# Kernel tuning notes

Measured on AMD Instinct MI355X. Metric: run time of the kernel, lower is better.

Reference implementation:

```python
import jax, jax.numpy as jnp
import numpy as np


def binarize(t):
    # sign binarizer to exactly +/-1 (sign(0) -> +1), matching is_binary_tensor check
    return jnp.where(t >= 0, 1.0, -1.0).astype(t.dtype)


def setup_inputs() -> dict:
    key = jax.random.key(0)
    kx, kw, kb = jax.random.split(key, 3)
    x = jax.random.normal(kx, (32, 256, 56, 56), dtype=jnp.float32)
    weight = jax.random.normal(kw, (256, 256, 3, 3), dtype=jnp.float32)
    bias = jax.random.normal(kb, (256,), dtype=jnp.float32)
    return {"x": x, "weight": weight, "bias": bias}


def reference(x, weight, bias):
    bx = binarize(x)            # [B, Cin, H, W] in {-1, +1}
    bw = binarize(weight)       # [Cout, Cin, kh, kw] in {-1, +1}
    # F.conv2d(stride=1, padding=1, dilation=1, groups=1)
    out = jax.lax.conv_general_dilated(
        bx, bw,
        window_strides=(1, 1),
        padding=((1, 1), (1, 1)),
        dimension_numbers=("NCHW", "OIHW", "NCHW"),
    )
    return out + bias[None, :, None, None]
```

## Files before the change

kernel.cpp:

```cpp
#include <hip/hip_runtime.h>
#include <cstdint>

constexpr int B = 32, C = 256, H = 56, W = 56;
constexpr int HW = H * W;
constexpr int WORDS = C / 32;
constexpr int TAPS = 9;
constexpr int WPC = TAPS * WORDS;
constexpr int PH = H + 2, PW = W + 2, PHW = PH * PW;

__global__ __launch_bounds__(256) void pack_x_kernel(const float* __restrict__ x,
                                                     uint32_t* __restrict__ px) {
    int idx = blockIdx.x * 256 + threadIdx.x;
    int pp = idx % PHW;
    int r = idx / PHW;
    int wd = r % WORDS;
    int b = r / WORDS;
    int ph = pp / PW, pwp = pp - ph * PW;
    uint32_t bits = 0;
    if (ph >= 1 && ph <= H && pwp >= 1 && pwp <= W) {
        const float* xp = x + ((size_t)b * C + wd * 32) * HW + (size_t)(ph - 1) * W + (pwp - 1);
        #pragma unroll
        for (int i = 0; i < 32; ++i)
            bits |= (xp[(size_t)i * HW] < 0.0f ? (1u << i) : 0u);
    }
    px[((size_t)(b * PH + ph) * PW + pwp) * WORDS + wd] = bits;
}

__global__ __launch_bounds__(256) void pack_w_kernel(const float* __restrict__ wt,
                                                     const float* __restrict__ bias,
                                                     uint32_t* __restrict__ pw,
                                                     float* __restrict__ basep) {
    int idx = blockIdx.x * 256 + threadIdx.x;
    if (idx < C) basep[idx] = 2304.0f + bias[idx];
    if (idx >= C * WPC) return;
    int co = idx / WPC;
    int r = idx - co * WPC;
    int tap = r / WORDS;
    int wd = r - tap * WORDS;
    const float* wp = wt + ((size_t)co * C + wd * 32) * TAPS + tap;
    uint32_t bits = 0;
    #pragma unroll
    for (int i = 0; i < 32; ++i)
        bits |= (wp[(size_t)i * TAPS] < 0.0f ? (1u << i) : 0u);
    pw[(size_t)co * WPC + (size_t)tap * WORDS + wd] = bits;
}

__global__ __launch_bounds__(256) void bconv_kernel(const uint32_t* __restrict__ px,
                                                    const uint32_t* __restrict__ pw,
                                                    const float* __restrict__ basep,
                                                    float* __restrict__ out) {
    const int lane = threadIdx.x & 63;
    const int wid = __builtin_amdgcn_readfirstlane(threadIdx.x >> 6);
    const int hw = blockIdx.x * 64 + lane;
    const int b = blockIdx.y;
    const int h = hw / W;
    const int w = hw - h * W;

    uint32_t pxr[TAPS][WORDS];
    #pragma unroll
    for (int dh = -1; dh <= 1; ++dh) {
        #pragma unroll
        for (int dw = -1; dw <= 1; ++dw) {
            const int t = (dh + 1) * 3 + (dw + 1);
            const uint4* p = reinterpret_cast<const uint4*>(
                px + ((size_t)(b * PH + (h + 1 + dh)) * PW + (w + 1 + dw)) * WORDS);
            uint4 a = p[0], q = p[1];
            pxr[t][0] = a.x; pxr[t][1] = a.y; pxr[t][2] = a.z; pxr[t][3] = a.w;
            pxr[t][4] = q.x; pxr[t][5] = q.y; pxr[t][6] = q.z; pxr[t][7] = q.w;
        }
    }

    const int cobase = wid * 64;
    const uint32_t* wbase = pw + (size_t)cobase * WPC;
    const float* bbase = basep + cobase;
    float* op = out + ((size_t)b * C + cobase) * HW + hw;

    #pragma unroll 1
    for (int j = 0; j < 64; ++j) {
        const uint32_t* wr = wbase + (size_t)j * WPC;
        uint32_t acc[4] = {0u, 0u, 0u, 0u};
        #pragma unroll
        for (int t = 0; t < TAPS; ++t) {
            #pragma unroll
            for (int k = 0; k < WORDS; ++k)
                acc[(t * WORDS + k) & 3] += __popc(pxr[t][k] ^ wr[t * WORDS + k]);
        }
        uint32_t total = (acc[0] + acc[1]) + (acc[2] + acc[3]);
        float res = fmaf(-2.0f, (float)(int)total, bbase[j]);
        op[(size_t)j * HW] = res;
    }
}

__global__ __launch_bounds__(256) void border_kernel(const uint32_t* __restrict__ px,
                                                     const uint32_t* __restrict__ pw,
                                                     const float* __restrict__ bias,
                                                     float* __restrict__ out) {
    int idx = blockIdx.x * 256 + threadIdx.x;
    int e = idx % 220;
    int r = idx / 220;
    int co = r & 255;
    int b = r >> 8;
    int h, w;
    if (e < 56)       { h = 0;            w = e; }
    else if (e < 112) { h = 55;           w = e - 56; }
    else if (e < 166) { h = 1 + (e - 112); w = 0; }
    else              { h = 1 + (e - 166); w = 55; }

    const uint32_t* wr = pw + (size_t)co * WPC;
    uint32_t total = 0;
    int nvalid = 0;
    #pragma unroll
    for (int dh = -1; dh <= 1; ++dh) {
        #pragma unroll
        for (int dw = -1; dw <= 1; ++dw) {
            const int t = (dh + 1) * 3 + (dw + 1);
            const int hh = h + dh, ww = w + dw;
            const bool v = (hh >= 0) & (hh < H) & (ww >= 0) & (ww < W);
            const uint32_t* p = px + ((size_t)(b * PH + (hh + 1)) * PW + (ww + 1)) * WORDS;
            uint32_t pt = 0;
            #pragma unroll
            for (int k = 0; k < WORDS; ++k)
                pt += __popc(p[k] ^ wr[t * WORDS + k]);
            total += v ? pt : 0u;
            nvalid += v ? 1 : 0;
        }
    }
    float res = (float)(256 * nvalid) - 2.0f * (float)(int)total + bias[co];
    out[((size_t)b * C + co) * HW + (size_t)h * W + w] = res;
}

extern "C" void kernel_launch(void* const* d_in, const int* in_sizes, int n_in,
                              void* d_out, int out_size, void* d_ws, size_t ws_size,
                              hipStream_t stream) {
    const float* x = (const float*)d_in[0];
    const float* wt = (const float*)d_in[1];
    const float* bias = (const float*)d_in[2];
    float* out = (float*)d_out;

    uint32_t* px = (uint32_t*)d_ws;
    uint32_t* pw = px + (size_t)B * PHW * WORDS;
    float* basep = (float*)(pw + (size_t)C * WPC);

    pack_x_kernel<<<(B * WORDS * PHW) / 256, 256, 0, stream>>>(x, px);
    pack_w_kernel<<<(C * WPC + 255) / 256, 256, 0, stream>>>(wt, bias, pw, basep);

    dim3 grid(HW / 64, B);
    bconv_kernel<<<grid, 256, 0, stream>>>(px, pw, basep, out);

    border_kernel<<<(B * C * 220) / 256, 256, 0, stream>>>(px, pw, bias, out);
}
```

Baseline: 382.9 us.

## Fold border padding correction into per-class bias table, drop border kernel

Padded pixels pack to zero bits, so the main kernel's XOR-popcount over all 9 taps overcounts at image borders by exactly the weight popcount of the out-of-bounds taps. A small kernel now precomputes, for each of the 9 boundary classes and each output channel, a constant of valid-tap count, invalid-tap weight popcount and bias. The main kernel picks its constant by pixel class, so the separate border kernel that recomputed border pixels is no longer needed. Weight packing also switches to a wave-wide ballot per 64 input channels instead of 32 strided loads per thread. This adds one tiny launch and a class lookup per thread.

```diff
diff --git a/kernel.cpp b/kernel.cpp
--- a/kernel.cpp
+++ b/kernel.cpp
@@ -27,27 +27,52 @@
 }
 
 __global__ __launch_bounds__(256) void pack_w_kernel(const float* __restrict__ wt,
-                                                     const float* __restrict__ bias,
-                                                     uint32_t* __restrict__ pw,
-                                                     float* __restrict__ basep) {
+                                                     uint32_t* __restrict__ pw) {
+    int gid = blockIdx.x * 256 + threadIdx.x;
+    int lane = gid & 63;
+    int wv = gid >> 6;
+    int pr = wv & 3;
+    int ct = wv >> 2;
+    int tap = ct % 9;
+    int co = ct / 9;
+    int ci = pr * 64 + lane;
+    float v = wt[((size_t)co * C + ci) * TAPS + tap];
+    unsigned long long m = __ballot(v < 0.0f);
+    if (lane == 0) {
+        pw[(size_t)co * WPC + tap * WORDS + pr * 2]     = (uint32_t)m;
+        pw[(size_t)co * WPC + tap * WORDS + pr * 2 + 1] = (uint32_t)(m >> 32);
+    }
+}
+
+__global__ __launch_bounds__(256) void basec_kernel(const uint32_t* __restrict__ pw,
+                                                    const float* __restrict__ bias,
+                                                    float* __restrict__ basec) {
     int idx = blockIdx.x * 256 + threadIdx.x;
-    if (idx < C) basep[idx] = 2304.0f + bias[idx];
-    if (idx >= C * WPC) return;
-    int co = idx / WPC;
-    int r = idx - co * WPC;
-    int tap = r / WORDS;
-    int wd = r - tap * WORDS;
-    const float* wp = wt + ((size_t)co * C + wd * 32) * TAPS + tap;
-    uint32_t bits = 0;
+    int co = idx & (C - 1);
+    int cls = idx >> 8;
+    int clsh = cls / 3, clsw = cls - clsh * 3;
+    int nvalid = 0, invsum = 0;
     #pragma unroll
-    for (int i = 0; i < 32; ++i)
-        bits |= (wp[(size_t)i * TAPS] < 0.0f ? (1u << i) : 0u);
-    pw[(size_t)co * WPC + (size_t)tap * WORDS + wd] = bits;
+    for (int t = 0; t < TAPS; ++t) {
+        int dh = t / 3 - 1, dw = t % 3 - 1;
+        bool vh = !((dh == -1 && clsh == 0) || (dh == 1 && clsh == 2));
+        bool vw = !((dw == -1 && clsw == 0) || (dw == 1 && clsw == 2));
+        if (vh && vw) {
+            ++nvalid;
+        } else {
+            int p = 0;
+            #pragma unroll
+            for (int k = 0; k < WORDS; ++k)
+                p += __popc(pw[(size_t)co * WPC + t * WORDS + k]);
+            invsum += p;
+        }
+    }
+    basec[idx] = (float)(256 * nvalid + 2 * invsum) + bias[co];
 }
 
 __global__ __launch_bounds__(256) void bconv_kernel(const uint32_t* __restrict__ px,
                                                     const uint32_t* __restrict__ pw,
-                                                    const float* __restrict__ basep,
+                                                    const float* __restrict__ basec,
                                                     float* __restrict__ out) {
     const int lane = threadIdx.x & 63;
     const int wid = __builtin_amdgcn_readfirstlane(threadIdx.x >> 6);
@@ -58,75 +83,40 @@
 
     uint32_t pxr[TAPS][WORDS];
     #pragma unroll
-    for (int dh = -1; dh <= 1; ++dh) {
-        #pragma unroll
-        for (int dw = -1; dw <= 1; ++dw) {
-            const int t = (dh + 1) * 3 + (dw + 1);
-            const uint4* p = reinterpret_cast<const uint4*>(
-                px + ((size_t)(b * PH + (h + 1 + dh)) * PW + (w + 1 + dw)) * WORDS);
-            uint4 a = p[0], q = p[1];
-            pxr[t][0] = a.x; pxr[t][1] = a.y; pxr[t][2] = a.z; pxr[t][3] = a.w;
-            pxr[t][4] = q.x; pxr[t][5] = q.y; pxr[t][6] = q.z; pxr[t][7] = q.w;
-        }
+    for (int t = 0; t < TAPS; ++t) {
+        const int dh = t / 3 - 1, dw = t - (t / 3) * 3 - 1;
+        const uint4* p = reinterpret_cast<const uint4*>(
+            px + ((size_t)(b * PH + (h + 1 + dh)) * PW + (w + 1 + dw)) * WORDS);
+        uint4 a = p[0], q = p[1];
+        pxr[t][0] = a.x; pxr[t][1] = a.y; pxr[t][2] = a.z; pxr[t][3] = a.w;
+        pxr[t][4] = q.x; pxr[t][5] = q.y; pxr[t][6] = q.z; pxr[t][7] = q.w;
     }
 
+    const int clsh = (h == 0) ? 0 : ((h == H - 1) ? 2 : 1);
+    const int clsw = (w == 0) ? 0 : ((w == W - 1) ? 2 : 1);
     const int cobase = wid * 64;
+    const float* bp = basec + (clsh * 3 + clsw) * C + cobase;
     const uint32_t* wbase = pw + (size_t)cobase * WPC;
-    const float* bbase = basep + cobase;
     float* op = out + ((size_t)b * C + cobase) * HW + hw;
 
     #pragma unroll 1
     for (int j = 0; j < 64; ++j) {
         const uint32_t* wr = wbase + (size_t)j * WPC;
-        uint32_t acc[4] = {0u, 0u, 0u, 0u};
+        uint32_t a0 = 0, a1 = 0, a2 = 0, a3 = 0;
         #pragma unroll
         for (int t = 0; t < TAPS; ++t) {
-            #pragma unroll
-            for (int k = 0; k < WORDS; ++k)
-                acc[(t * WORDS + k) & 3] += __popc(pxr[t][k] ^ wr[t * WORDS + k]);
+            a0 += __popc(pxr[t][0] ^ wr[t * WORDS + 0]);
+            a1 += __popc(pxr[t][1] ^ wr[t * WORDS + 1]);
+            a2 += __popc(pxr[t][2] ^ wr[t * WORDS + 2]);
+            a3 += __popc(pxr[t][3] ^ wr[t * WORDS + 3]);
+            a0 += __popc(pxr[t][4] ^ wr[t * WORDS + 4]);
+            a1 += __popc(pxr[t][5] ^ wr[t * WORDS + 5]);
+            a2 += __popc(pxr[t][6] ^ wr[t * WORDS + 6]);
+            a3 += __popc(pxr[t][7] ^ wr[t * WORDS + 7]);
         }
-        uint32_t total = (acc[0] + acc[1]) + (acc[2] + acc[3]);
-        float res = fmaf(-2.0f, (float)(int)total, bbase[j]);
-        op[(size_t)j * HW] = res;
+        uint32_t total = (a0 + a1) + (a2 + a3);
+        op[(size_t)j * HW] = fmaf(-2.0f, (float)(int)total, bp[j]);
     }
-}
-
-__global__ __launch_bounds__(256) void border_kernel(const uint32_t* __restrict__ px,
-                                                     const uint32_t* __restrict__ pw,
-                                                     const float* __restrict__ bias,
-                                                     float* __restrict__ out) {
-    int idx = blockIdx.x * 256 + threadIdx.x;
-    int e = idx % 220;
-    int r = idx / 220;
-    int co = r & 255;
-    int b = r >> 8;
-    int h, w;
-    if (e < 56)       { h = 0;            w = e; }
-    else if (e < 112) { h = 55;           w = e - 56; }
-    else if (e < 166) { h = 1 + (e - 112); w = 0; }
-    else              { h = 1 + (e - 166); w = 55; }
-
-    const uint32_t* wr = pw + (size_t)co * WPC;
-    uint32_t total = 0;
-    int nvalid = 0;
-    #pragma unroll
-    for (int dh = -1; dh <= 1; ++dh) {
-        #pragma unroll
-        for (int dw = -1; dw <= 1; ++dw) {
-            const int t = (dh + 1) * 3 + (dw + 1);
-            const int hh = h + dh, ww = w + dw;
-            const bool v = (hh >= 0) & (hh < H) & (ww >= 0) & (ww < W);
-            const uint32_t* p = px + ((size_t)(b * PH + (hh + 1)) * PW + (ww + 1)) * WORDS;
-            uint32_t pt = 0;
-            #pragma unroll
-            for (int k = 0; k < WORDS; ++k)
-                pt += __popc(p[k] ^ wr[t * WORDS + k]);
-            total += v ? pt : 0u;
-            nvalid += v ? 1 : 0;
-        }
-    }
-    float res = (float)(256 * nvalid) - 2.0f * (float)(int)total + bias[co];
-    out[((size_t)b * C + co) * HW + (size_t)h * W + w] = res;
 }
 
 extern "C" void kernel_launch(void* const* d_in, const int* in_sizes, int n_in,
@@ -139,13 +129,12 @@
 
     uint32_t* px = (uint32_t*)d_ws;
     uint32_t* pw = px + (size_t)B * PHW * WORDS;
-    float* basep = (float*)(pw + (size_t)C * WPC);
+    float* basec = (float*)(pw + (size_t)C * WPC);
 
     pack_x_kernel<<<(B * WORDS * PHW) / 256, 256, 0, stream>>>(x, px);
-    pack_w_kernel<<<(C * WPC + 255) / 256, 256, 0, stream>>>(wt, bias, pw, basep);
+    pack_w_kernel<<<(C * TAPS * 4 * 64) / 256, 256, 0, stream>>>(wt, pw);
+    basec_kernel<<<(9 * C) / 256, 256, 0, stream>>>(pw, bias, basec);
 
     dim3 grid(HW / 64, B);
-    bconv_kernel<<<grid, 256, 0, stream>>>(px, pw, basep, out);
-
-    border_kernel<<<(B * C * 220) / 256, 256, 0, stream>>>(px, pw, bias, out);
+    bconv_kernel<<<grid, 256, 0, stream>>>(px, pw, basec, out);
 }
```

New measurement: 387.3 us. About the same (+1.2%).
